# Kernel tuning notes

Hardware: AMD Instinct MI355X
Metric: run time of the kernel (lower is better)

## Reference

```python
import jax, jax.numpy as jnp
import numpy as np

B, S, D, T = 64, 1024, 768, 10
IS = int(S * 0.3)   # 307, token-mix inner dim
ID = int(D * 0.3)   # 230, channel-mix inner dim
EPS = 1e-5


def _cond_ln(x, embed, tid):
    # LayerNorm over last dim (no affine), then per-sample gamma/beta
    mu = jnp.mean(x, axis=-1, keepdims=True)
    var = jnp.mean(jnp.square(x - mu), axis=-1, keepdims=True)
    out = (x - mu) / jnp.sqrt(var + EPS)
    gb = embed[tid]                      # [B, 2D]
    gamma, beta = gb[:, :D], gb[:, D:]
    return gamma[:, None, :] * out + beta[:, None, :]


def setup_inputs() -> dict:
    key = jax.random.key(0)
    ks = jax.random.split(key, 8)
    x = jax.random.normal(ks[0], (B, S, D), dtype=jnp.float32)
    tasks_id = jax.random.randint(ks[1], (B,), 0, T)
    # conditional LN embeddings: gamma ~ N(1, 0.02), beta = 0
    cln1 = jnp.concatenate([1.0 + 0.02 * jax.random.normal(ks[2], (T, D)),
                            jnp.zeros((T, D))], axis=1).astype(jnp.float32)
    cln2 = jnp.concatenate([1.0 + 0.02 * jax.random.normal(ks[3], (T, D)),
                            jnp.zeros((T, D))], axis=1).astype(jnp.float32)
    # per-task weights stored [T, fout, fin] (kaiming-ish scale)
    w1_tok = jax.random.normal(ks[4], (T, IS, S), dtype=jnp.float32) * (2.0 / S) ** 0.5
    w2_tok = jax.random.normal(ks[5], (T, S, IS), dtype=jnp.float32) * (2.0 / IS) ** 0.5
    w1_ch = jax.random.normal(ks[6], (T, ID, D), dtype=jnp.float32) * (2.0 / D) ** 0.5
    w2_ch = jax.random.normal(ks[7], (T, D, ID), dtype=jnp.float32) * (2.0 / ID) ** 0.5
    return {"x": x, "tasks_id": tasks_id, "cln1": cln1, "cln2": cln2,
            "w1_tok": w1_tok, "w2_tok": w2_tok, "w1_ch": w1_ch, "w2_ch": w2_ch}


def reference(x, tasks_id, cln1, cln2, w1_tok, w2_tok, w1_ch, w2_ch):
    tid = tasks_id
    # --- token-mixing block (axis=1 ConditionalLinear) ---
    h = _cond_ln(x, cln1, tid)
    h = jnp.einsum('bnd,bcn->bcd', h, w1_tok[tid])   # [B, IS, D]
    h = jax.nn.gelu(h, approximate=False)
    h = jnp.einsum('bnd,bcn->bcd', h, w2_tok[tid])   # [B, S, D]
    x = x + h
    # --- channel-mixing block (axis=2 ConditionalLinear) ---
    h = _cond_ln(x, cln2, tid)
    h = jnp.einsum('bnd,bcd->bnc', h, w1_ch[tid])    # [B, S, ID]
    h = jax.nn.gelu(h, approximate=False)
    h = jnp.einsum('bnd,bcd->bnc', h, w2_ch[tid])    # [B, S, D]
    x = x + h
    return x
```

## Files before the change

kernel.cpp:

```cpp
#include <hip/hip_runtime.h>
#include <math.h>

typedef __bf16 bf16x8 __attribute__((ext_vector_type(8)));
typedef __bf16 bf16x4 __attribute__((ext_vector_type(4)));
typedef float  f32x4  __attribute__((ext_vector_type(4)));

constexpr int Bc = 64, Sc = 1024, Dc = 768;
constexpr int ISc = 307, IDc = 230;
constexpr int ISp = 384, IDp = 256;

static __device__ __forceinline__ float bf2f(unsigned short u) {
    return __builtin_bit_cast(float, (unsigned)u << 16);
}
static __device__ __forceinline__ float gelu_f(float v) {
    const float y = v * (0.7978845608f + 0.0356774081f * v * v);
    const float e = __builtin_amdgcn_exp2f(y * 2.8853900818f);
    return v * e * __builtin_amdgcn_rcpf(e + 1.0f);
}

static __device__ __forceinline__ void gload16(const void* g, void* l) {
    __builtin_amdgcn_global_load_lds(
        (const __attribute__((address_space(1))) void*)g,
        (__attribute__((address_space(3))) void*)l, 16, 0, 0);
}

constexpr int CH0 = 10 * ISp * (Sc  / 8);
constexpr int CH1 = 10 * Sc  * (ISp / 8);
constexpr int CH2 = 10 * IDp * (Dc  / 8);
constexpr int CH3 = 10 * Dc  * (IDp / 8);
constexpr int CB0 = CH0, CB1 = CB0 + CH1, CB2 = CB1 + CH2, CB3 = CB2 + CH3;
constexpr int CVT_BLK = CB3 / 256;
constexpr int LN1_BLK = (Sc / 32) * Bc;

__device__ __forceinline__ void cvt_one(
    const float* __restrict__ in, __bf16* __restrict__ out,
    int inrows, int outrows, int incols, int outcols, int c)
{
    const int cpr  = outcols >> 3;
    const int perT = outrows * cpr;
    const int t    = c / perT;
    const int rem  = c - t * perT;
    const int r    = rem / cpr;
    const int cc   = (rem - r * cpr) * 8;
    bf16x8 o;
    if (r < inrows) {
        const float* src = in + ((long)t * inrows + r) * incols + cc;
        #pragma unroll
        for (int e = 0; e < 8; e++)
            o[e] = (cc + e < incols) ? (__bf16)src[e] : (__bf16)0.0f;
    } else {
        #pragma unroll
        for (int e = 0; e < 8; e++) o[e] = (__bf16)0.0f;
    }
    *reinterpret_cast<bf16x8*>(out + ((long)t * outrows + r) * outcols + cc) = o;
}

__global__ __launch_bounds__(256) void front_k(
    const float* __restrict__ w1t, const float* __restrict__ w2t,
    const float* __restrict__ w1c, const float* __restrict__ w2c,
    __bf16* __restrict__ o1t, __bf16* __restrict__ o2t,
    __bf16* __restrict__ o1c, __bf16* __restrict__ o2c,
    const float* __restrict__ x, const int* __restrict__ tasks,
    const float* __restrict__ cln, __bf16* __restrict__ h1T)
{
    constexpr int RPB = 32, LDT = Dc + 8;
    __shared__ unsigned short T[RPB * LDT];
    const int bid = blockIdx.x;
    if (bid < CVT_BLK) {
        const int c = bid * 256 + threadIdx.x;
        if (c < CB0)      cvt_one(w1t, o1t, ISc, ISp, Sc,  Sc,  c);
        else if (c < CB1) cvt_one(w2t, o2t, Sc,  Sc,  ISc, ISp, c - CB0);
        else if (c < CB2) cvt_one(w1c, o1c, IDc, IDp, Dc,  Dc,  c - CB1);
        else              cvt_one(w2c, o2c, Dc,  Dc,  IDc, IDp, c - CB2);
        return;
    }
    const int idx = bid - CVT_BLK;
    const int b   = idx >> 5;
    const int s0  = (idx & 31) * RPB;
    const int t   = tasks[b];
    const int tid = threadIdx.x;
    const int wv  = tid >> 6;
    const int l   = tid & 63;

    const float4* Ga = reinterpret_cast<const float4*>(cln + (long)t * 2 * Dc);
    const float4* Be = reinterpret_cast<const float4*>(cln + (long)t * 2 * Dc + Dc);
    const float4 g0 = Ga[l], g1 = Ga[l + 64], g2 = Ga[l + 128];
    const float4 b0 = Be[l], b1 = Be[l + 64], b2 = Be[l + 128];

    #pragma unroll
    for (int rr = 0; rr < 8; rr++) {
        const int r = wv * 8 + rr;
        const float4* xr = reinterpret_cast<const float4*>(x + ((long)b * Sc + s0 + r) * Dc);
        const float4 v0 = xr[l], v1 = xr[l + 64], v2 = xr[l + 128];
        float s = v0.x + v0.y + v0.z + v0.w + v1.x + v1.y + v1.z + v1.w
                + v2.x + v2.y + v2.z + v2.w;
        float q = v0.x*v0.x + v0.y*v0.y + v0.z*v0.z + v0.w*v0.w
                + v1.x*v1.x + v1.y*v1.y + v1.z*v1.z + v1.w*v1.w
                + v2.x*v2.x + v2.y*v2.y + v2.z*v2.z + v2.w*v2.w;
        #pragma unroll
        for (int o = 1; o < 64; o <<= 1) { s += __shfl_xor(s, o); q += __shfl_xor(q, o); }
        const float mu   = s * (1.0f / Dc);
        const float var  = fmaxf(q * (1.0f / Dc) - mu * mu, 0.0f);
        const float rstd = 1.0f / sqrtf(var + 1e-5f);
        unsigned short* tr = &T[r * LDT];
        bf16x4 o0, o1, o2;
        o0[0] = (__bf16)(g0.x * ((v0.x - mu) * rstd) + b0.x);
        o0[1] = (__bf16)(g0.y * ((v0.y - mu) * rstd) + b0.y);
        o0[2] = (__bf16)(g0.z * ((v0.z - mu) * rstd) + b0.z);
        o0[3] = (__bf16)(g0.w * ((v0.w - mu) * rstd) + b0.w);
        o1[0] = (__bf16)(g1.x * ((v1.x - mu) * rstd) + b1.x);
        o1[1] = (__bf16)(g1.y * ((v1.y - mu) * rstd) + b1.y);
        o1[2] = (__bf16)(g1.z * ((v1.z - mu) * rstd) + b1.z);
        o1[3] = (__bf16)(g1.w * ((v1.w - mu) * rstd) + b1.w);
        o2[0] = (__bf16)(g2.x * ((v2.x - mu) * rstd) + b2.x);
        o2[1] = (__bf16)(g2.y * ((v2.y - mu) * rstd) + b2.y);
        o2[2] = (__bf16)(g2.z * ((v2.z - mu) * rstd) + b2.z);
        o2[3] = (__bf16)(g2.w * ((v2.w - mu) * rstd) + b2.w);
        *reinterpret_cast<bf16x4*>(&tr[l * 4])        = o0;
        *reinterpret_cast<bf16x4*>(&tr[256 + l * 4])  = o1;
        *reinterpret_cast<bf16x4*>(&tr[512 + l * 4])  = o2;
    }
    __syncthreads();
    #pragma unroll
    for (int c = 0; c < 3; c++) {
        const int d = tid + c * 256;
        unsigned short tmp[32];
        #pragma unroll
        for (int e = 0; e < 32; e++) tmp[e] = T[e * LDT + d];
        __bf16* dst = h1T + ((long)b * Dc + d) * Sc + s0;
        #pragma unroll
        for (int u = 0; u < 4; u++)
            reinterpret_cast<uint4*>(dst)[u] = reinterpret_cast<const uint4*>(tmp)[u];
    }
}

template<int DOGELU, int RESM, int OUTF32, int ATASK>
__global__ __launch_bounds__(512, 4) void gemm_tn(
    const __bf16* __restrict__ A, long sA, int lda,
    const __bf16* __restrict__ B, long sB, int ldb,
    const void* __restrict__ R, long sR,
    void* __restrict__ C, long sC, int ldc,
    const int* __restrict__ tasks, int M, int N, int K)
{
    constexpr int BM = 128, BN = 128, BK = 64;
    constexpr int BUFB = 32768;
    __shared__ uint4 lds4[2 * BUFB / 16];
    char* lbase = (char*)lds4;

    const int gx  = gridDim.x, gy = gridDim.y;
    const int tpb = gx * gy;
    const long lin = blockIdx.x + (long)gx * (blockIdx.y + (long)gy * blockIdx.z);
    const int  xcd  = (int)(lin & 7);
    const long idx  = lin >> 3;
    const int  lb   = (int)(idx / tpb);
    const int  tile = (int)(idx - (long)lb * tpb);
    const int  b    = xcd * 8 + lb;
    const int  m0   = (tile / gx) * BM;
    const int  n0   = (tile % gx) * BN;

    const int t = tasks[b];
    const __bf16* Ab = A + (ATASK ? (long)t : (long)b) * sA;
    const __bf16* Bb = B + (ATASK ? (long)b : (long)t) * sB;
    const int tid = threadIdx.x, lane = tid & 63, wid = tid >> 6;
    const int wm = (wid >> 1) * 32, wn = (wid & 1) * 64;
    const int l15 = lane & 15, l4 = lane >> 4;

    f32x4 acc[2][4];
    #pragma unroll
    for (int i = 0; i < 2; i++)
        #pragma unroll
        for (int j = 0; j < 4; j++)
            acc[i][j] = (f32x4){0.f, 0.f, 0.f, 0.f};

    auto STAGE = [&](int k0, int buf) {
        char* dst = lbase + buf * BUFB;
        #pragma unroll
        for (int rep = 0; rep < 2; rep++) {
            const int c = rep * 512 + tid;
            const int m = c >> 3, ch = c & 7;
            const int gk = k0 + ((ch ^ (m & 7)) << 3);
            gload16(Ab + (long)(m0 + m) * lda + gk, dst + c * 16);
        }
        #pragma unroll
        for (int rep = 0; rep < 2; rep++) {
            const int c = rep * 512 + tid;
            const int n = c >> 3, ch = c & 7;
            const int gk = k0 + ((ch ^ (n & 7)) << 3);
            gload16(Bb + (long)(n0 + n) * ldb + gk, dst + 16384 + c * 16);
        }
    };

    const int nt = K / BK;
    STAGE(0, 0);
    __syncthreads();
    int cur = 0;
    for (int tt = 0; tt < nt; tt++) {
        if (tt + 1 < nt) STAGE((tt + 1) * BK, cur ^ 1);
        const char* bb = lbase + cur * BUFB;
        #pragma unroll
        for (int h = 0; h < 2; h++) {
            bf16x8 af[2], bfr[4];
            #pragma unroll
            for (int i = 0; i < 2; i++) {
                const int row = wm + i * 16 + l15;
                af[i] = *reinterpret_cast<const bf16x8*>(
                    bb + row * 128 + (((h * 4 + l4) ^ (row & 7)) << 4));
            }
            #pragma unroll
            for (int j = 0; j < 4; j++) {
                const int row = wn + j * 16 + l15;
                bfr[j] = *reinterpret_cast<const bf16x8*>(
                    bb + 16384 + row * 128 + (((h * 4 + l4) ^ (row & 7)) << 4));
            }
            #pragma unroll
            for (int i = 0; i < 2; i++)
                #pragma unroll
                for (int j = 0; j < 4; j++)
                    acc[i][j] = __builtin_amdgcn_mfma_f32_16x16x32_bf16(af[i], bfr[j], acc[i][j], 0, 0, 0);
        }
        __syncthreads();
        cur ^= 1;
    }

    float*  Cf = (float*)C  + (long)b * sC;
    __bf16* Ch = (__bf16*)C + (long)b * sC;
    const float*  Rf = (RESM == 1) ? ((const float*)R  + (long)b * sR) : nullptr;
    const __bf16* Rh = (RESM == 2) ? ((const __bf16*)R + (long)b * sR) : nullptr;

    #pragma unroll
    for (int i = 0; i < 2; i++) {
        #pragma unroll
        for (int j = 0; j < 4; j++) {
            const int gn = n0 + wn + j * 16 + l15;
            #pragma unroll
            for (int r = 0; r < 4; r++) {
                const int gm = m0 + wm + i * 16 + l4 * 4 + r;
                float v = acc[i][j][r];
                if (DOGELU) v = gelu_f(v);
                if (RESM == 1) v += Rf[(long)gm * ldc + gn];
                if (RESM == 2) v += (float)Rh[(long)gm * ldc + gn];
                if (OUTF32) Cf[(long)gm * ldc + gn] = v;
                else        Ch[(long)gm * ldc + gn] = (__bf16)v;
            }
        }
    }
}

__global__ __launch_bounds__(512, 4) void mlp_ch(
    const __bf16* __restrict__ x1, const int* __restrict__ tasks,
    const float* __restrict__ cln2,
    const __bf16* __restrict__ wC1,
    const __bf16* __restrict__ wC2,
    float* __restrict__ out)
{
    __shared__ float2 st[64];
    __shared__ unsigned short G[64 * 256];
    __shared__ char sbuf[2][20480];

    const int lin = blockIdx.x;
    const int xcd = lin & 7;
    const int idx = lin >> 3;
    const int b   = xcd * 8 + (idx >> 4);
    const int m0  = (idx & 15) * 64;
    const int t   = tasks[b];

    const int tid = threadIdx.x;
    const int wid = tid >> 6, lane = tid & 63;
    const int wm  = (wid >> 2) * 32, wn = (wid & 3) * 64;
    const int l15 = lane & 15, l4 = lane >> 4;

    const __bf16* xb = x1 + ((long)b * Sc + m0) * Dc;
    const float*  cg = cln2 + (long)t * 2 * Dc;
    const float*  cb = cg + Dc;

    #pragma unroll 2
    for (int rr = 0; rr < 8; rr++) {
        const int m = wid * 8 + rr;
        const ushort4* xr = reinterpret_cast<const ushort4*>(xb + (long)m * Dc);
        const ushort4 u0 = xr[lane], u1 = xr[lane + 64], u2 = xr[lane + 128];
        float s = 0.f, q = 0.f, v;
        v = bf2f(u0.x); s += v; q += v*v;  v = bf2f(u0.y); s += v; q += v*v;
        v = bf2f(u0.z); s += v; q += v*v;  v = bf2f(u0.w); s += v; q += v*v;
        v = bf2f(u1.x); s += v; q += v*v;  v = bf2f(u1.y); s += v; q += v*v;
        v = bf2f(u1.z); s += v; q += v*v;  v = bf2f(u1.w); s += v; q += v*v;
        v = bf2f(u2.x); s += v; q += v*v;  v = bf2f(u2.y); s += v; q += v*v;
        v = bf2f(u2.z); s += v; q += v*v;  v = bf2f(u2.w); s += v; q += v*v;
        #pragma unroll
        for (int o = 1; o < 64; o <<= 1) { s += __shfl_xor(s, o); q += __shfl_xor(q, o); }
        if (lane == 0) {
            const float mu  = s * (1.0f / Dc);
            const float var = fmaxf(q * (1.0f / Dc) - mu * mu, 0.0f);
            st[m] = make_float2(mu, 1.0f / sqrtf(var + 1e-5f));
        }
    }
    __syncthreads();

    const int am = tid >> 3, ach8 = tid & 7;
    const float2 ams = st[am];
    const __bf16* arow = xb + (long)am * Dc;

    auto loadA = [&](int kt) -> bf16x4 {
        return *reinterpret_cast<const bf16x4*>(arow + kt * 32 + ach8 * 4);
    };
    auto writeA = [&](bf16x4 a, int buf) {
        const int phys = (ach8 >> 1) ^ ((am >> 1) & 3);
        *reinterpret_cast<bf16x4*>(
            sbuf[buf] + am * 64 + (phys << 4) + (ach8 & 1) * 8) = a;
    };
    auto stageB1 = [&](int kt, int buf) {
        #pragma unroll
        for (int rep = 0; rep < 2; rep++) {
            const int c = rep * 512 + tid;
            const int n = c >> 2, ch = c & 3;
            const int gk = kt * 32 + ((ch ^ ((n >> 1) & 3)) << 3);
            gload16(wC1 + ((long)t * IDp + n) * Dc + gk, sbuf[buf] + 4096 + c * 16);
        }
    };
    auto xformA = [&](bf16x4 raw, int kt) -> bf16x4 {
        const int gk = kt * 32 + ach8 * 4;
        const float4 ga = *reinterpret_cast<const float4*>(cg + gk);
        const float4 be = *reinterpret_cast<const float4*>(cb + gk);
        bf16x4 o;
        o[0] = (__bf16)(ga.x * ((float)raw[0] - ams.x) * ams.y + be.x);
        o[1] = (__bf16)(ga.y * ((float)raw[1] - ams.x) * ams.y + be.y);
        o[2] = (__bf16)(ga.z * ((float)raw[2] - ams.x) * ams.y + be.z);
        o[3] = (__bf16)(ga.w * ((float)raw[3] - ams.x) * ams.y + be.w);
        return o;
    };
    const __bf16* w2b = wC2 + (long)t * Dc * IDp;
    auto stageB2 = [&](int nc, int kt, int buf) {
        #pragma unroll
        for (int rep = 0; rep < 2; rep++) {
            const int c = rep * 512 + tid;
            const int n = c >> 2, ch = c & 3;
            const int gk = kt * 32 + ((ch ^ ((n >> 1) & 3)) << 3);
            gload16(w2b + (long)(nc * 256 + n) * IDp + gk, sbuf[buf] + c * 16);
        }
    };

    f32x4 acc[2][4];
    #pragma unroll
    for (int i = 0; i < 2; i++)
        #pragma unroll
        for (int j = 0; j < 4; j++)
            acc[i][j] = (f32x4){0.f, 0.f, 0.f, 0.f};

    {
        bf16x4 a0 = loadA(0);
        stageB1(0, 0);
        writeA(xformA(a0, 0), 0);
        __syncthreads();
        for (int kt = 0; kt < 24; kt++) {
            const int buf = kt & 1;
            bf16x4 anx;
            if (kt < 23) { anx = loadA(kt + 1); stageB1(kt + 1, buf ^ 1); }
            const char* Abase = sbuf[buf];
            const char* Bbase = sbuf[buf] + 4096;
            bf16x8 af[2], bfr[4];
            #pragma unroll
            for (int i = 0; i < 2; i++) {
                const int row = wm + i * 16 + l15;
                af[i] = *reinterpret_cast<const bf16x8*>(
                    Abase + row * 64 + ((l4 ^ ((row >> 1) & 3)) << 4));
            }
            #pragma unroll
            for (int j = 0; j < 4; j++) {
                const int row = wn + j * 16 + l15;
                bfr[j] = *reinterpret_cast<const bf16x8*>(
                    Bbase + row * 64 + ((l4 ^ ((row >> 1) & 3)) << 4));
            }
            #pragma unroll
            for (int i = 0; i < 2; i++)
                #pragma unroll
                for (int j = 0; j < 4; j++)
                    acc[i][j] = __builtin_amdgcn_mfma_f32_16x16x32_bf16(af[i], bfr[j], acc[i][j], 0, 0, 0);
            if (kt < 23) writeA(xformA(anx, kt + 1), buf ^ 1);
            __syncthreads();
        }
    }

    stageB2(0, 0, 0);

    #pragma unroll
    for (int i = 0; i < 2; i++) {
        #pragma unroll
        for (int j = 0; j < 4; j++) {
            const int k = wn + j * 16 + l15;
            #pragma unroll
            for (int r = 0; r < 4; r++) {
                const int m = wm + i * 16 + l4 * 4 + r;
                const float v = gelu_f(acc[i][j][r]);
                const int phys = (k >> 3) ^ (m & 7);
                G[m * 256 + phys * 8 + (k & 7)] =
                    __builtin_bit_cast(unsigned short, (__bf16)v);
            }
        }
    }
    __syncthreads();

    float* ob = out + ((long)b * Sc + m0) * Dc;
    for (int nc = 0; nc < 3; nc++) {
        f32x4 a2[2][4];
        #pragma unroll
        for (int i = 0; i < 2; i++)
            #pragma unroll
            for (int j = 0; j < 4; j++)
                a2[i][j] = (f32x4){0.f, 0.f, 0.f, 0.f};

        float res[2][4][4];
        #pragma unroll
        for (int i = 0; i < 2; i++)
            #pragma unroll
            for (int j = 0; j < 4; j++) {
                const int gn = nc * 256 + wn + j * 16 + l15;
                #pragma unroll
                for (int r = 0; r < 4; r++) {
                    const int gm = wm + i * 16 + l4 * 4 + r;
                    res[i][j][r] = (float)xb[(long)gm * Dc + gn];
                }
            }

        for (int kt = 0; kt < 8; kt++) {
            const int buf = kt & 1;
            if (kt < 7)       stageB2(nc, kt + 1, buf ^ 1);
            else if (nc < 2)  stageB2(nc + 1, 0, buf ^ 1);
            bf16x8 af[2], bfr[4];
            #pragma unroll
            for (int i = 0; i < 2; i++) {
                const int row = wm + i * 16 + l15;
                const int phys = (kt * 4 + l4) ^ (row & 7);
                af[i] = *reinterpret_cast<const bf16x8*>(
                    (const char*)G + row * 512 + phys * 16);
            }
            #pragma unroll
            for (int j = 0; j < 4; j++) {
                const int row = wn + j * 16 + l15;
                bfr[j] = *reinterpret_cast<const bf16x8*>(
                    sbuf[buf] + row * 64 + ((l4 ^ ((row >> 1) & 3)) << 4));
            }
            #pragma unroll
            for (int i = 0; i < 2; i++)
                #pragma unroll
                for (int j = 0; j < 4; j++)
                    a2[i][j] = __builtin_amdgcn_mfma_f32_16x16x32_bf16(af[i], bfr[j], a2[i][j], 0, 0, 0);
            __syncthreads();
        }
        #pragma unroll
        for (int i = 0; i < 2; i++) {
            #pragma unroll
            for (int j = 0; j < 4; j++) {
                const int gn = nc * 256 + wn + j * 16 + l15;
                #pragma unroll
                for (int r = 0; r < 4; r++) {
                    const int gm = wm + i * 16 + l4 * 4 + r;
                    ob[(long)gm * Dc + gn] = a2[i][j][r] + res[i][j][r];
                }
            }
        }
    }
}

extern "C" void kernel_launch(void* const* d_in, const int* in_sizes, int n_in,
                              void* d_out, int out_size, void* d_ws, size_t ws_size,
                              hipStream_t stream) {
    const float* x      = (const float*)d_in[0];
    const int*   tasks  = (const int*)  d_in[1];
    const float* cln1   = (const float*)d_in[2];
    const float* cln2   = (const float*)d_in[3];
    const float* w1_tok = (const float*)d_in[4];
    const float* w2_tok = (const float*)d_in[5];
    const float* w1_ch  = (const float*)d_in[6];
    const float* w2_ch  = (const float*)d_in[7];
    float* out = (float*)d_out;

    char* ws = (char*)d_ws;
    const long oT1 = 0;
    const long oT2 = oT1 + (long)10 * ISp * Sc * 2;
    const long oC1 = oT2 + (long)10 * Sc * ISp * 2;
    const long oC2 = oC1 + (long)10 * IDp * Dc * 2;
    const long oA  = oC2 + (long)10 * Dc * IDp * 2;
    const long oG  = oA  + (long)Bc * Dc * Sc * 2;
    __bf16* wT1  = (__bf16*)(ws + oT1);
    __bf16* wT2  = (__bf16*)(ws + oT2);
    __bf16* wC1  = (__bf16*)(ws + oC1);
    __bf16* wC2  = (__bf16*)(ws + oC2);
    __bf16* h1T  = (__bf16*)(ws + oA);
    __bf16* x1   = (__bf16*)(ws + oA);
    __bf16* gbf  = (__bf16*)(ws + oG);

    front_k<<<CVT_BLK + LN1_BLK, 256, 0, stream>>>(
        w1_tok, w2_tok, w1_ch, w2_ch, wT1, wT2, wC1, wC2,
        x, tasks, cln1, h1T);

    gemm_tn<1, 0, 0, 0><<<dim3(ISp / 128, Dc / 128, Bc), 512, 0, stream>>>(
        h1T, (long)Dc * Sc, Sc,
        wT1, (long)ISp * Sc, Sc,
        nullptr, 0,
        gbf, (long)Dc * ISp, ISp,
        tasks, Dc, ISp, Sc);

    gemm_tn<0, 1, 0, 1><<<dim3(Dc / 128, Sc / 128, Bc), 512, 0, stream>>>(
        wT2, (long)Sc * ISp, ISp,
        gbf, (long)Dc * ISp, ISp,
        x, (long)Sc * Dc,
        x1, (long)Sc * Dc, Dc,
        tasks, Sc, Dc, ISp);

    mlp_ch<<<(Sc / 64) * Bc, 512, 0, stream>>>(x1, tasks, cln2, wC1, wC2, out);
}
```

Measured before the change: 404.6 us.

## Fold channel-LN affine into W1 and apply normalization in GEMM epilogue

Folds the cond-LN gamma of the channel-mixing block into the bf16 W1 conversion and precomputes per-task vectors u=W1·gamma and v=W1·beta in extra front-kernel blocks. The mlp_ch first GEMM then streams raw x1 tiles into LDS via direct global-to-LDS loads instead of loading, normalizing and writing them through registers. Normalization is applied in the epilogue as rstd*acc - rstd*mu*u + v. This removes per-element LN work and the register round-trip from the GEMM main loop. The cost is a few extra front blocks and slightly different rounding, since the raw bf16 x1 is multiplied before mean subtraction.

New measurement: 382.8 us. 5.4% less time.

```diff
diff --git a/kernel.cpp b/kernel.cpp
--- a/kernel.cpp
+++ b/kernel.cpp
@@ -31,6 +31,7 @@
 constexpr int CB0 = CH0, CB1 = CB0 + CH1, CB2 = CB1 + CH2, CB3 = CB2 + CH3;
 constexpr int CVT_BLK = CB3 / 256;
 constexpr int LN1_BLK = (Sc / 32) * Bc;
+constexpr int UV_BLK  = (10 * 256) / 4;
 
 __device__ __forceinline__ void cvt_one(
     const float* __restrict__ in, __bf16* __restrict__ out,
@@ -61,7 +62,9 @@
     __bf16* __restrict__ o1t, __bf16* __restrict__ o2t,
     __bf16* __restrict__ o1c, __bf16* __restrict__ o2c,
     const float* __restrict__ x, const int* __restrict__ tasks,
-    const float* __restrict__ cln, __bf16* __restrict__ h1T)
+    const float* __restrict__ cln1, const float* __restrict__ cln2,
+    __bf16* __restrict__ h1T,
+    float* __restrict__ uvu, float* __restrict__ uvv)
 {
     constexpr int RPB = 32, LDT = Dc + 8;
     __shared__ unsigned short T[RPB * LDT];
@@ -70,68 +73,109 @@
         const int c = bid * 256 + threadIdx.x;
         if (c < CB0)      cvt_one(w1t, o1t, ISc, ISp, Sc,  Sc,  c);
         else if (c < CB1) cvt_one(w2t, o2t, Sc,  Sc,  ISc, ISp, c - CB0);
-        else if (c < CB2) cvt_one(w1c, o1c, IDc, IDp, Dc,  Dc,  c - CB1);
+        else if (c < CB2) {
+            const int c2  = c - CB1;
+            const int cpr = Dc >> 3;
+            const int perT = IDp * cpr;
+            const int t   = c2 / perT;
+            const int rem = c2 - t * perT;
+            const int r   = rem / cpr;
+            const int cc  = (rem - r * cpr) * 8;
+            bf16x8 o;
+            if (r < IDc) {
+                const float* src = w1c + ((long)t * IDc + r) * Dc + cc;
+                const float* gsr = cln2 + (long)t * 2 * Dc + cc;
+                #pragma unroll
+                for (int e = 0; e < 8; e++)
+                    o[e] = (__bf16)(src[e] * gsr[e]);
+            } else {
+                #pragma unroll
+                for (int e = 0; e < 8; e++) o[e] = (__bf16)0.0f;
+            }
+            *reinterpret_cast<bf16x8*>(o1c + ((long)t * IDp + r) * Dc + cc) = o;
+        }
         else              cvt_one(w2c, o2c, Dc,  Dc,  IDc, IDp, c - CB2);
         return;
     }
-    const int idx = bid - CVT_BLK;
-    const int b   = idx >> 5;
-    const int s0  = (idx & 31) * RPB;
-    const int t   = tasks[b];
-    const int tid = threadIdx.x;
-    const int wv  = tid >> 6;
-    const int l   = tid & 63;
-
-    const float4* Ga = reinterpret_cast<const float4*>(cln + (long)t * 2 * Dc);
-    const float4* Be = reinterpret_cast<const float4*>(cln + (long)t * 2 * Dc + Dc);
-    const float4 g0 = Ga[l], g1 = Ga[l + 64], g2 = Ga[l + 128];
-    const float4 b0 = Be[l], b1 = Be[l + 64], b2 = Be[l + 128];
-
+    if (bid < CVT_BLK + LN1_BLK) {
+        const int idx = bid - CVT_BLK;
+        const int b   = idx >> 5;
+        const int s0  = (idx & 31) * RPB;
+        const int t   = tasks[b];
+        const int tid = threadIdx.x;
+        const int wv  = tid >> 6;
+        const int l   = tid & 63;
+
+        const float4* Ga = reinterpret_cast<const float4*>(cln1 + (long)t * 2 * Dc);
+        const float4* Be = reinterpret_cast<const float4*>(cln1 + (long)t * 2 * Dc + Dc);
+        const float4 g0 = Ga[l], g1 = Ga[l + 64], g2 = Ga[l + 128];
+        const float4 b0 = Be[l], b1 = Be[l + 64], b2 = Be[l + 128];
+
+        #pragma unroll
+        for (int rr = 0; rr < 8; rr++) {
+            const int r = wv * 8 + rr;
+            const float4* xr = reinterpret_cast<const float4*>(x + ((long)b * Sc + s0 + r) * Dc);
+            const float4 v0 = xr[l], v1 = xr[l + 64], v2 = xr[l + 128];
+            float s = v0.x + v0.y + v0.z + v0.w + v1.x + v1.y + v1.z + v1.w
+                    + v2.x + v2.y + v2.z + v2.w;
+            float q = v0.x*v0.x + v0.y*v0.y + v0.z*v0.z + v0.w*v0.w
+                    + v1.x*v1.x + v1.y*v1.y + v1.z*v1.z + v1.w*v1.w
+                    + v2.x*v2.x + v2.y*v2.y + v2.z*v2.z + v2.w*v2.w;
+            #pragma unroll
+            for (int o = 1; o < 64; o <<= 1) { s += __shfl_xor(s, o); q += __shfl_xor(q, o); }
+            const float mu   = s * (1.0f / Dc);
+            const float var  = fmaxf(q * (1.0f / Dc) - mu * mu, 0.0f);
+            const float rstd = 1.0f / sqrtf(var + 1e-5f);
+            unsigned short* tr = &T[r * LDT];
+            bf16x4 o0, o1, o2;
+            o0[0] = (__bf16)(g0.x * ((v0.x - mu) * rstd) + b0.x);
+            o0[1] = (__bf16)(g0.y * ((v0.y - mu) * rstd) + b0.y);
+            o0[2] = (__bf16)(g0.z * ((v0.z - mu) * rstd) + b0.z);
+            o0[3] = (__bf16)(g0.w * ((v0.w - mu) * rstd) + b0.w);
+            o1[0] = (__bf16)(g1.x * ((v1.x - mu) * rstd) + b1.x);
+            o1[1] = (__bf16)(g1.y * ((v1.y - mu) * rstd) + b1.y);
+            o1[2] = (__bf16)(g1.z * ((v1.z - mu) * rstd) + b1.z);
+            o1[3] = (__bf16)(g1.w * ((v1.w - mu) * rstd) + b1.w);
+            o2[0] = (__bf16)(g2.x * ((v2.x - mu) * rstd) + b2.x);
+            o2[1] = (__bf16)(g2.y * ((v2.y - mu) * rstd) + b2.y);
+            o2[2] = (__bf16)(g2.z * ((v2.z - mu) * rstd) + b2.z);
+            o2[3] = (__bf16)(g2.w * ((v2.w - mu) * rstd) + b2.w);
+            *reinterpret_cast<bf16x4*>(&tr[l * 4])        = o0;
+            *reinterpret_cast<bf16x4*>(&tr[256 + l * 4])  = o1;
+            *reinterpret_cast<bf16x4*>(&tr[512 + l * 4])  = o2;
+        }
+        __syncthreads();
+        #pragma unroll
+        for (int c = 0; c < 3; c++) {
+            const int d = threadIdx.x + c * 256;
+            unsigned short tmp[32];
+            #pragma unroll
+            for (int e = 0; e < 32; e++) tmp[e] = T[e * LDT + d];
+            __bf16* dst = h1T + ((long)b * Dc + d) * Sc + s0;
+            #pragma unroll
+            for (int u = 0; u < 4; u++)
+                reinterpret_cast<uint4*>(dst)[u] = reinterpret_cast<const uint4*>(tmp)[u];
+        }
+        return;
+    }
+    const int p = (bid - CVT_BLK - LN1_BLK) * 4 + (threadIdx.x >> 6);
+    const int t = p >> 8, n = p & 255;
+    const int l = threadIdx.x & 63;
+    float su = 0.f, sv = 0.f;
+    if (n < IDc) {
+        const float* wr = w1c + ((long)t * IDc + n) * Dc + l * 12;
+        const float* gr = cln2 + (long)t * 2 * Dc + l * 12;
+        const float* br = gr + Dc;
+        #pragma unroll
+        for (int e = 0; e < 12; e++) {
+            const float w = wr[e];
+            su += gr[e] * w;
+            sv += br[e] * w;
+        }
+    }
     #pragma unroll
-    for (int rr = 0; rr < 8; rr++) {
-        const int r = wv * 8 + rr;
-        const float4* xr = reinterpret_cast<const float4*>(x + ((long)b * Sc + s0 + r) * Dc);
-        const float4 v0 = xr[l], v1 = xr[l + 64], v2 = xr[l + 128];
-        float s = v0.x + v0.y + v0.z + v0.w + v1.x + v1.y + v1.z + v1.w
-                + v2.x + v2.y + v2.z + v2.w;
-        float q = v0.x*v0.x + v0.y*v0.y + v0.z*v0.z + v0.w*v0.w
-                + v1.x*v1.x + v1.y*v1.y + v1.z*v1.z + v1.w*v1.w
-                + v2.x*v2.x + v2.y*v2.y + v2.z*v2.z + v2.w*v2.w;
-        #pragma unroll
-        for (int o = 1; o < 64; o <<= 1) { s += __shfl_xor(s, o); q += __shfl_xor(q, o); }
-        const float mu   = s * (1.0f / Dc);
-        const float var  = fmaxf(q * (1.0f / Dc) - mu * mu, 0.0f);
-        const float rstd = 1.0f / sqrtf(var + 1e-5f);
-        unsigned short* tr = &T[r * LDT];
-        bf16x4 o0, o1, o2;
-        o0[0] = (__bf16)(g0.x * ((v0.x - mu) * rstd) + b0.x);
-        o0[1] = (__bf16)(g0.y * ((v0.y - mu) * rstd) + b0.y);
-        o0[2] = (__bf16)(g0.z * ((v0.z - mu) * rstd) + b0.z);
-        o0[3] = (__bf16)(g0.w * ((v0.w - mu) * rstd) + b0.w);
-        o1[0] = (__bf16)(g1.x * ((v1.x - mu) * rstd) + b1.x);
-        o1[1] = (__bf16)(g1.y * ((v1.y - mu) * rstd) + b1.y);
-        o1[2] = (__bf16)(g1.z * ((v1.z - mu) * rstd) + b1.z);
-        o1[3] = (__bf16)(g1.w * ((v1.w - mu) * rstd) + b1.w);
-        o2[0] = (__bf16)(g2.x * ((v2.x - mu) * rstd) + b2.x);
-        o2[1] = (__bf16)(g2.y * ((v2.y - mu) * rstd) + b2.y);
-        o2[2] = (__bf16)(g2.z * ((v2.z - mu) * rstd) + b2.z);
-        o2[3] = (__bf16)(g2.w * ((v2.w - mu) * rstd) + b2.w);
-        *reinterpret_cast<bf16x4*>(&tr[l * 4])        = o0;
-        *reinterpret_cast<bf16x4*>(&tr[256 + l * 4])  = o1;
-        *reinterpret_cast<bf16x4*>(&tr[512 + l * 4])  = o2;
-    }
-    __syncthreads();
-    #pragma unroll
-    for (int c = 0; c < 3; c++) {
-        const int d = tid + c * 256;
-        unsigned short tmp[32];
-        #pragma unroll
-        for (int e = 0; e < 32; e++) tmp[e] = T[e * LDT + d];
-        __bf16* dst = h1T + ((long)b * Dc + d) * Sc + s0;
-        #pragma unroll
-        for (int u = 0; u < 4; u++)
-            reinterpret_cast<uint4*>(dst)[u] = reinterpret_cast<const uint4*>(tmp)[u];
-    }
+    for (int o = 1; o < 64; o <<= 1) { su += __shfl_xor(su, o); sv += __shfl_xor(sv, o); }
+    if (l == 0) { uvu[t * 256 + n] = su; uvv[t * 256 + n] = sv; }
 }
 
 template<int DOGELU, int RESM, int OUTF32, int ATASK>
@@ -248,7 +292,7 @@
 
 __global__ __launch_bounds__(512, 4) void mlp_ch(
     const __bf16* __restrict__ x1, const int* __restrict__ tasks,
-    const float* __restrict__ cln2,
+    const float* __restrict__ uvu, const float* __restrict__ uvv,
     const __bf16* __restrict__ wC1,
     const __bf16* __restrict__ wC2,
     float* __restrict__ out)
@@ -270,8 +314,6 @@
     const int l15 = lane & 15, l4 = lane >> 4;
 
     const __bf16* xb = x1 + ((long)b * Sc + m0) * Dc;
-    const float*  cg = cln2 + (long)t * 2 * Dc;
-    const float*  cb = cg + Dc;
 
     #pragma unroll 2
     for (int rr = 0; rr < 8; rr++) {
@@ -295,17 +337,12 @@
     }
     __syncthreads();
 
-    const int am = tid >> 3, ach8 = tid & 7;
-    const float2 ams = st[am];
-    const __bf16* arow = xb + (long)am * Dc;
-
-    auto loadA = [&](int kt) -> bf16x4 {
-        return *reinterpret_cast<const bf16x4*>(arow + kt * 32 + ach8 * 4);
-    };
-    auto writeA = [&](bf16x4 a, int buf) {
-        const int phys = (ach8 >> 1) ^ ((am >> 1) & 3);
-        *reinterpret_cast<bf16x4*>(
-            sbuf[buf] + am * 64 + (phys << 4) + (ach8 & 1) * 8) = a;
+    auto stageA = [&](int kt, int buf) {
+        if (tid < 256) {
+            const int m = tid >> 2, ch = tid & 3;
+            const int gk = kt * 32 + ((ch ^ ((m >> 1) & 3)) << 3);
+            gload16(xb + (long)m * Dc + gk, sbuf[buf] + tid * 16);
+        }
     };
     auto stageB1 = [&](int kt, int buf) {
         #pragma unroll
@@ -316,17 +353,6 @@
             gload16(wC1 + ((long)t * IDp + n) * Dc + gk, sbuf[buf] + 4096 + c * 16);
         }
     };
-    auto xformA = [&](bf16x4 raw, int kt) -> bf16x4 {
-        const int gk = kt * 32 + ach8 * 4;
-        const float4 ga = *reinterpret_cast<const float4*>(cg + gk);
-        const float4 be = *reinterpret_cast<const float4*>(cb + gk);
-        bf16x4 o;
-        o[0] = (__bf16)(ga.x * ((float)raw[0] - ams.x) * ams.y + be.x);
-        o[1] = (__bf16)(ga.y * ((float)raw[1] - ams.x) * ams.y + be.y);
-        o[2] = (__bf16)(ga.z * ((float)raw[2] - ams.x) * ams.y + be.z);
-        o[3] = (__bf16)(ga.w * ((float)raw[3] - ams.x) * ams.y + be.w);
-        return o;
-    };
     const __bf16* w2b = wC2 + (long)t * Dc * IDp;
     auto stageB2 = [&](int nc, int kt, int buf) {
         #pragma unroll
@@ -345,51 +371,56 @@
         for (int j = 0; j < 4; j++)
             acc[i][j] = (f32x4){0.f, 0.f, 0.f, 0.f};
 
-    {
-        bf16x4 a0 = loadA(0);
-        stageB1(0, 0);
-        writeA(xformA(a0, 0), 0);
+    stageA(0, 0);
+    stageB1(0, 0);
+    __syncthreads();
+    for (int kt = 0; kt < 24; kt++) {
+        const int buf = kt & 1;
+        if (kt < 23) { stageA(kt + 1, buf ^ 1); stageB1(kt + 1, buf ^ 1); }
+        const char* Abase = sbuf[buf];
+        const char* Bbase = sbuf[buf] + 4096;
+        bf16x8 af[2], bfr[4];
+        #pragma unroll
+        for (int i = 0; i < 2; i++) {
+            const int row = wm + i * 16 + l15;
+            af[i] = *reinterpret_cast<const bf16x8*>(
+                Abase + row * 64 + ((l4 ^ ((row >> 1) & 3)) << 4));
+        }
+        #pragma unroll
+        for (int j = 0; j < 4; j++) {
+            const int row = wn + j * 16 + l15;
+            bfr[j] = *reinterpret_cast<const bf16x8*>(
+                Bbase + row * 64 + ((l4 ^ ((row >> 1) & 3)) << 4));
+        }
+        #pragma unroll
+        for (int i = 0; i < 2; i++)
+            #pragma unroll
+            for (int j = 0; j < 4; j++)
+                acc[i][j] = __builtin_amdgcn_mfma_f32_16x16x32_bf16(af[i], bfr[j], acc[i][j], 0, 0, 0);
         __syncthreads();
-        for (int kt = 0; kt < 24; kt++) {
-            const int buf = kt & 1;
-            bf16x4 anx;
-            if (kt < 23) { anx = loadA(kt + 1); stageB1(kt + 1, buf ^ 1); }
-            const char* Abase = sbuf[buf];
-            const char* Bbase = sbuf[buf] + 4096;
-            bf16x8 af[2], bfr[4];
-            #pragma unroll
-            for (int i = 0; i < 2; i++) {
-                const int row = wm + i * 16 + l15;
-                af[i] = *reinterpret_cast<const bf16x8*>(
-                    Abase + row * 64 + ((l4 ^ ((row >> 1) & 3)) << 4));
-            }
-            #pragma unroll
-            for (int j = 0; j < 4; j++) {
-                const int row = wn + j * 16 + l15;
-                bfr[j] = *reinterpret_cast<const bf16x8*>(
-                    Bbase + row * 64 + ((l4 ^ ((row >> 1) & 3)) << 4));
-            }
-            #pragma unroll
-            for (int i = 0; i < 2; i++)
-                #pragma unroll
-                for (int j = 0; j < 4; j++)
-                    acc[i][j] = __builtin_amdgcn_mfma_f32_16x16x32_bf16(af[i], bfr[j], acc[i][j], 0, 0, 0);
-            if (kt < 23) writeA(xformA(anx, kt + 1), buf ^ 1);
-            __syncthreads();
-        }
     }
 
     stageB2(0, 0, 0);
 
+    float uu[4], vv[4];
+    #pragma unroll
+    for (int j = 0; j < 4; j++) {
+        const int gn = wn + j * 16 + l15;
+        uu[j] = uvu[t * 256 + gn];
+        vv[j] = uvv[t * 256 + gn];
+    }
     #pragma unroll
     for (int i = 0; i < 2; i++) {
         #pragma unroll
-        for (int j = 0; j < 4; j++) {
-            const int k = wn + j * 16 + l15;
-            #pragma unroll
-            for (int r = 0; r < 4; r++) {
-                const int m = wm + i * 16 + l4 * 4 + r;
-                const float v = gelu_f(acc[i][j][r]);
+        for (int r = 0; r < 4; r++) {
+            const int m = wm + i * 16 + l4 * 4 + r;
+            const float2 smr = st[m];
+            const float rs = smr.y, rmu = smr.y * smr.x;
+            #pragma unroll
+            for (int j = 0; j < 4; j++) {
+                const int k = wn + j * 16 + l15;
+                const float pre = rs * acc[i][j][r] - rmu * uu[j] + vv[j];
+                const float v = gelu_f(pre);
                 const int phys = (k >> 3) ^ (m & 7);
                 G[m * 256 + phys * 8 + (k & 7)] =
                     __builtin_bit_cast(unsigned short, (__bf16)v);
@@ -478,19 +509,23 @@
     const long oT2 = oT1 + (long)10 * ISp * Sc * 2;
     const long oC1 = oT2 + (long)10 * Sc * ISp * 2;
     const long oC2 = oC1 + (long)10 * IDp * Dc * 2;
-    const long oA  = oC2 + (long)10 * Dc * IDp * 2;
+    const long oU  = oC2 + (long)10 * Dc * IDp * 2;
+    const long oV  = oU  + (long)10 * 256 * 4;
+    const long oA  = oV  + (long)10 * 256 * 4;
     const long oG  = oA  + (long)Bc * Dc * Sc * 2;
     __bf16* wT1  = (__bf16*)(ws + oT1);
     __bf16* wT2  = (__bf16*)(ws + oT2);
     __bf16* wC1  = (__bf16*)(ws + oC1);
     __bf16* wC2  = (__bf16*)(ws + oC2);
+    float*  uvu  = (float*)(ws + oU);
+    float*  uvv  = (float*)(ws + oV);
     __bf16* h1T  = (__bf16*)(ws + oA);
     __bf16* x1   = (__bf16*)(ws + oA);
     __bf16* gbf  = (__bf16*)(ws + oG);
 
-    front_k<<<CVT_BLK + LN1_BLK, 256, 0, stream>>>(
+    front_k<<<CVT_BLK + LN1_BLK + UV_BLK, 256, 0, stream>>>(
         w1_tok, w2_tok, w1_ch, w2_ch, wT1, wT2, wC1, wC2,
-        x, tasks, cln1, h1T);
+        x, tasks, cln1, cln2, h1T, uvu, uvv);
 
     gemm_tn<1, 0, 0, 0><<<dim3(ISp / 128, Dc / 128, Bc), 512, 0, stream>>>(
         h1T, (long)Dc * Sc, Sc,
@@ -506,5 +541,5 @@
         x1, (long)Sc * Dc, Dc,
         tasks, Sc, Dc, ISp);
 
-    mlp_ch<<<(Sc / 64) * Bc, 512, 0, stream>>>(x1, tasks, cln2, wC1, wC2, out);
-}
+    mlp_ch<<<(Sc / 64) * Bc, 512, 0, stream>>>(x1, tasks, uvu, uvv, wC1, wC2, out);
+}
```
